# Kernel optimization log

Measured on AMD Instinct MI355X. Metric: run time of the kernel, lower is better.

The kernel has to match this reference:

```python
import jax, jax.numpy as jnp
import numpy as np

# dims
B, L, HID, TDIM, LT = 8, 4096, 1024, 768, 77
DIM = 512            # vmamba_dim
D_INNER = 2 * DIM    # expand = 2
NHEADS = DIM // 16   # 32
HEADDIM = D_INNER // NHEADS  # 32
D_STATE = 64
CONV_K = 4
CONV_DIM = D_INNER + 2 * D_STATE  # 1152
D_PROJ = 2 * D_INNER + 2 * D_STATE + NHEADS  # z | xBC | dt


def setup_inputs() -> dict:
    key = jax.random.key(0)
    ks = jax.random.split(key, 20)
    s = 0.02
    return {
        "image_tokens": jax.random.normal(ks[0], (B, L, HID), jnp.float32),
        "text_tokens": jax.random.normal(ks[1], (B, LT, TDIM), jnp.float32),
        "W_in": jax.random.normal(ks[2], (HID, DIM), jnp.float32) * s,
        "b_in": jnp.zeros((DIM,), jnp.float32),
        "W_txt": jax.random.normal(ks[3], (TDIM, DIM), jnp.float32) * s,
        "b_txt": jnp.zeros((DIM,), jnp.float32),
        "norm_w": jnp.ones((DIM,), jnp.float32),
        "norm_b": jnp.zeros((DIM,), jnp.float32),
        "W_zxbcdt": jax.random.normal(ks[4], (DIM, D_PROJ), jnp.float32) * s,
        "b_zxbcdt": jnp.zeros((D_PROJ,), jnp.float32),
        "conv_w": jax.random.normal(ks[5], (CONV_DIM, CONV_K), jnp.float32) * 0.1,
        "conv_b": jnp.zeros((CONV_DIM,), jnp.float32),
        "dt_bias": jax.random.uniform(ks[6], (NHEADS,), jnp.float32, -4.0, -2.0),
        "A_log": jnp.log(jnp.arange(1, NHEADS + 1, dtype=jnp.float32)),
        "D": jnp.ones((NHEADS,), jnp.float32),
        "W_blk_out": jax.random.normal(ks[7], (D_INNER, DIM), jnp.float32) * s,
        "b_blk_out": jnp.zeros((DIM,), jnp.float32),
        "W_out": jax.random.normal(ks[8], (DIM, HID), jnp.float32) * s,
        "b_out": jnp.zeros((HID,), jnp.float32),
    }


def _layernorm(x, w, b, eps=1e-5):
    mu = x.mean(-1, keepdims=True)
    var = ((x - mu) ** 2).mean(-1, keepdims=True)
    return (x - mu) * jax.lax.rsqrt(var + eps) * w + b


def _mamba2_block(tok, norm_w, norm_b, W_zxbcdt, b_zxbcdt, conv_w, conv_b,
                  dt_bias, A_log, Dp, W_blk_out, b_blk_out):
    x = _layernorm(tok, norm_w, norm_b)
    zxbcdt = x @ W_zxbcdt + b_zxbcdt                       # [B,L,D_PROJ]
    z = zxbcdt[..., :D_INNER]
    xBC = zxbcdt[..., D_INNER:D_INNER + CONV_DIM]
    dt = zxbcdt[..., D_INNER + CONV_DIM:]                  # [B,L,H]
    # causal depthwise conv1d, kernel 4
    xp = jnp.pad(xBC, ((0, 0), (CONV_K - 1, 0), (0, 0)))
    conv = sum(xp[:, k:k + L, :] * conv_w[None, None, :, k] for k in range(CONV_K))
    xBC = jax.nn.silu(conv + conv_b)
    xh = xBC[..., :D_INNER].reshape(B, L, NHEADS, HEADDIM)  # [B,L,H,P]
    Bm = xBC[..., D_INNER:D_INNER + D_STATE]                # [B,L,N]
    Cm = xBC[..., D_INNER + D_STATE:]                       # [B,L,N]
    dt = jax.nn.softplus(dt + dt_bias)                      # [B,L,H]
    A = -jnp.exp(A_log)                                     # [H]
    dA = jnp.exp(dt * A)                                    # [B,L,H]

    def step(h, xs):
        dA_t, dt_t, B_t, C_t, x_t = xs   # [B,H],[B,H],[B,N],[B,N],[B,H,P]
        h = h * dA_t[:, :, None, None] + \
            (dt_t[:, :, None, None] * x_t[..., None]) * B_t[:, None, None, :]
        y = jnp.einsum('bhpn,bn->bhp', h, C_t)
        return h, y

    xs = (dA.transpose(1, 0, 2), dt.transpose(1, 0, 2),
          Bm.transpose(1, 0, 2), Cm.transpose(1, 0, 2),
          xh.transpose(1, 0, 2, 3))
    h0 = jnp.zeros((B, NHEADS, HEADDIM, D_STATE), tok.dtype)
    _, ys = jax.lax.scan(step, h0, xs)                      # [L,B,H,P]
    y = ys.transpose(1, 0, 2, 3) + Dp[None, None, :, None] * xh
    y = y.reshape(B, L, D_INNER) * jax.nn.silu(z)
    return tok + (y @ W_blk_out + b_blk_out)                # residual


def reference(image_tokens, text_tokens, W_in, b_in, W_txt, b_txt,
              norm_w, norm_b, W_zxbcdt, b_zxbcdt, conv_w, conv_b,
              dt_bias, A_log, D, W_blk_out, b_blk_out, W_out, b_out):
    txt = text_tokens[:, 0, :] @ W_txt + b_txt              # cls pool
    tok = image_tokens @ W_in + b_in + txt[:, None, :]
    tok = _mamba2_block(tok, norm_w, norm_b, W_zxbcdt, b_zxbcdt, conv_w,
                        conv_b, dt_bias, A_log, D, W_blk_out, b_blk_out)
    tok = tok @ W_out + b_out                               # [B,L,HID]
    return tok.mean(axis=1)                                 # AdaptiveAvgPool1d(1)
```

## Files before the change

### kernel.cpp

```cpp
#include <hip/hip_runtime.h>

typedef unsigned short U16;
typedef __attribute__((ext_vector_type(2))) float f32x2;
typedef __attribute__((ext_vector_type(4))) float f32x4;
typedef __attribute__((ext_vector_type(8))) short short8;
typedef __attribute__((ext_vector_type(8))) __bf16 bf16x8;

#define Bsz 8
#define Lsz 4096
#define HID 1024
#define DIMV 512
#define D_INNER 1024
#define NHEADS 32
#define HEADDIM 32
#define D_STATE 64
#define CONV_DIM 1152
#define D_PROJ 2208
#define D_PROJ_PAD 2304
#define MROWS 32768
#define CL2 512
#define NSUB 8
#define NCH 8

__device__ __forceinline__ float bf2f(U16 u) {
  return __builtin_bit_cast(float, (unsigned)(((unsigned)u) << 16));
}
__device__ __forceinline__ U16 f2bf(float f) {
  unsigned u = __builtin_bit_cast(unsigned, f);
  return (U16)((u + 0x7FFFu + ((u >> 16) & 1u)) >> 16);
}
__device__ __forceinline__ void gload_lds16(const void* g, void* l) {
  __builtin_amdgcn_global_load_lds((const __attribute__((address_space(1))) unsigned int*)g,
                                   (__attribute__((address_space(3))) unsigned int*)l, 16, 0, 0);
}

__global__ __launch_bounds__(512) void txt_kernel(const float* __restrict__ text,
                                                  const float* __restrict__ Wt,
                                                  const float* __restrict__ bt,
                                                  float* __restrict__ txt) {
  int b = blockIdx.x, j = threadIdx.x;
  float s = bt[j];
  const float* tp = text + (size_t)b * 77 * 768;
  for (int k = 0; k < 768; ++k) s += tp[k] * Wt[(size_t)k * 512 + j];
  txt[b * 512 + j] = s;
}

__global__ __launch_bounds__(256) void cvt_f2b_kernel(const float* __restrict__ in,
                                                      U16* __restrict__ out, int n4) {
  int i = blockIdx.x * 256 + threadIdx.x;
  if (i < n4) {
    float4 v = reinterpret_cast<const float4*>(in)[i];
    ushort4 o;
    o.x = f2bf(v.x); o.y = f2bf(v.y); o.z = f2bf(v.z); o.w = f2bf(v.w);
    reinterpret_cast<ushort4*>(out)[i] = o;
  }
}

__global__ __launch_bounds__(256) void transpose_cvt_kernel(const float* __restrict__ in,
                                                            U16* __restrict__ out,
                                                            int K, int N, int Npad) {
  __shared__ U16 tile[32][33];
  int n0 = blockIdx.x * 32, k0 = blockIdx.y * 32;
  int tx = threadIdx.x, ty = threadIdx.y;
  #pragma unroll
  for (int i = 0; i < 4; ++i) {
    int k = k0 + ty + i * 8, n = n0 + tx;
    float v = (n < N) ? in[(size_t)k * N + n] : 0.f;
    tile[ty + i * 8][tx] = f2bf(v);
  }
  __syncthreads();
  #pragma unroll
  for (int i = 0; i < 4; ++i) {
    int n = n0 + ty + i * 8;
    out[(size_t)n * K + k0 + tx] = tile[tx][ty + i * 8];
  }
}

template <int EPI>
__global__ __launch_bounds__(256) void gemm_kernel(const U16* __restrict__ A,
                                                   const U16* __restrict__ Bt,
                                                   U16* __restrict__ C,
                                                   const float* __restrict__ bias,
                                                   const float* __restrict__ txtv,
                                                   int M, int K, int Nreal) {
  __shared__ alignas(16) U16 As[128 * 64];
  __shared__ alignas(16) U16 Bs[128 * 64];
  const int tid = threadIdx.x;
  const int wid = tid >> 6, lane = tid & 63;
  const int lhi = lane >> 4, llo = lane & 15;
  const int m0 = blockIdx.x * 128;
  const int n0 = blockIdx.y * 128;
  const int wr = wid >> 1, wc = wid & 1;
  f32x4 acc[4][4] = {};

  for (int k0 = 0; k0 < K; k0 += 64) {
    __syncthreads();
    #pragma unroll
    for (int is = 0; is < 4; ++is) {
      int qbase = is * 256 + wid * 64;
      int q = qbase + lane;
      int r = q >> 3;
      int cc = (q & 7) ^ (r & 7);
      gload_lds16(A + (size_t)(m0 + r) * K + k0 + cc * 8, &As[qbase * 8]);
    }
    #pragma unroll
    for (int is = 0; is < 4; ++is) {
      int qbase = is * 256 + wid * 64;
      int q = qbase + lane;
      int r = q >> 3;
      int cc = (q & 7) ^ (r & 7);
      gload_lds16(Bt + (size_t)(n0 + r) * K + k0 + cc * 8, &Bs[qbase * 8]);
    }
    __syncthreads();
    #pragma unroll
    for (int kk = 0; kk < 64; kk += 32) {
      bf16x8 av[4], bv[4];
      #pragma unroll
      for (int i = 0; i < 4; ++i) {
        int ra = wr * 64 + i * 16 + llo;
        short8 a = *reinterpret_cast<const short8*>(
            &As[ra * 64 + ((((kk >> 3) + lhi) ^ (ra & 7)) << 3)]);
        av[i] = __builtin_bit_cast(bf16x8, a);
        int rb = wc * 64 + i * 16 + llo;
        short8 b = *reinterpret_cast<const short8*>(
            &Bs[rb * 64 + ((((kk >> 3) + lhi) ^ (rb & 7)) << 3)]);
        bv[i] = __builtin_bit_cast(bf16x8, b);
      }
      #pragma unroll
      for (int i = 0; i < 4; ++i)
        #pragma unroll
        for (int j = 0; j < 4; ++j)
          acc[i][j] = __builtin_amdgcn_mfma_f32_16x16x32_bf16(av[i], bv[j], acc[i][j], 0, 0, 0);
    }
  }
  const int b = m0 >> 12;
  #pragma unroll
  for (int i = 0; i < 4; ++i) {
    int rbase = m0 + wr * 64 + i * 16 + lhi * 4;
    #pragma unroll
    for (int j = 0; j < 4; ++j) {
      int cg = n0 + wc * 64 + j * 16 + llo;
      if (cg < Nreal) {
        float badd = bias[cg] + (EPI ? txtv[b * 512 + cg] : 0.f);
        #pragma unroll
        for (int r = 0; r < 4; ++r)
          C[(size_t)(rbase + r) * Nreal + cg] = f2bf(acc[i][j][r] + badd);
      }
    }
  }
}

__global__ __launch_bounds__(128) void ln_kernel(const U16* __restrict__ tok,
                                                 U16* __restrict__ xo,
                                                 const float* __restrict__ w,
                                                 const float* __restrict__ bb) {
  int row = blockIdx.x, tid = threadIdx.x;
  const U16* rp = tok + (size_t)row * 512 + tid * 4;
  uint2 raw = *reinterpret_cast<const uint2*>(rp);
  float f0 = bf2f((U16)(raw.x & 0xffff)), f1 = bf2f((U16)(raw.x >> 16));
  float f2 = bf2f((U16)(raw.y & 0xffff)), f3 = bf2f((U16)(raw.y >> 16));
  float s = f0 + f1 + f2 + f3;
  float q = f0 * f0 + f1 * f1 + f2 * f2 + f3 * f3;
  for (int m = 1; m < 64; m <<= 1) { s += __shfl_xor(s, m); q += __shfl_xor(q, m); }
  __shared__ float ss[2], qq[2];
  if ((tid & 63) == 0) { ss[tid >> 6] = s; qq[tid >> 6] = q; }
  __syncthreads();
  s = ss[0] + ss[1]; q = qq[0] + qq[1];
  float mu = s * (1.f / 512.f);
  float var = q * (1.f / 512.f) - mu * mu;
  float rs = rsqrtf(var + 1e-5f);
  int j0 = tid * 4;
  unsigned c0 = f2bf((f0 - mu) * rs * w[j0] + bb[j0]);
  unsigned c1 = f2bf((f1 - mu) * rs * w[j0 + 1] + bb[j0 + 1]);
  unsigned c2 = f2bf((f2 - mu) * rs * w[j0 + 2] + bb[j0 + 2]);
  unsigned c3 = f2bf((f3 - mu) * rs * w[j0 + 3] + bb[j0 + 3]);
  uint2 o; o.x = c0 | (c1 << 16); o.y = c2 | (c3 << 16);
  *reinterpret_cast<uint2*>(xo + (size_t)row * 512 + j0) = o;
}

__global__ __launch_bounds__(256) void tokpart_kernel(const U16* __restrict__ tok,
                                                      float* __restrict__ part) {
  int b = blockIdx.x, j = blockIdx.y * 256 + threadIdx.x, z = blockIdx.z;
  float s = 0.f;
  int l0 = z * 256;
  for (int l = l0; l < l0 + 256; ++l)
    s += bf2f(tok[((size_t)b * Lsz + l) * 512 + j]);
  part[(z * 8 + b) * 512 + j] = s;
}

__global__ __launch_bounds__(256) void dt_kernel(const U16* __restrict__ zx,
                                                 const float* __restrict__ dt_bias,
                                                 const float* __restrict__ A_log,
                                                 float* __restrict__ ldt2f,
                                                 float* __restrict__ ldA2f) {
  int idx = blockIdx.x * 256 + threadIdx.x;
  int row = idx >> 5, hh = idx & 31;
  float raw = bf2f(zx[(size_t)row * D_PROJ + 2176 + hh]) + dt_bias[hh];
  float dt = (raw > 20.f) ? raw : log1pf(__expf(raw));
  float A = -__expf(A_log[hh]);
  ldt2f[idx] = __log2f(dt);
  ldA2f[idx] = dt * A * 1.44269504088896f;
}

__global__ __launch_bounds__(256) void conv_tr_kernel(
    const U16* __restrict__ zx, const float* __restrict__ cw,
    const float* __restrict__ cb, U16* __restrict__ Bmo, U16* __restrict__ Cmo,
    U16* __restrict__ xh_t, U16* __restrict__ gz_t,
    U16* __restrict__ bm_t, U16* __restrict__ cm_t) {
  __shared__ U16 tile[64 * 72];
  const int lt = blockIdx.x, ct = blockIdx.y;
  const int r0 = lt * 64;
  const int b = r0 >> 12, l0 = r0 & 4095;
  const int tid = threadIdx.x;
  const int c = tid & 63, lqb = tid >> 6;

  if (ct < 16) {
    const int zc0 = ct * 64;
    #pragma unroll
    for (int it = 0; it < 4; ++it) {
      int lq4 = (lqb + it * 4) * 4;
      float v[4];
      #pragma unroll
      for (int j = 0; j < 4; ++j) {
        float z = bf2f(zx[(size_t)(r0 + lq4 + j) * D_PROJ + zc0 + c]);
        v[j] = z / (1.f + __expf(-z));
      }
      uint2 p2;
      p2.x = (unsigned)f2bf(v[0]) | ((unsigned)f2bf(v[1]) << 16);
      p2.y = (unsigned)f2bf(v[2]) | ((unsigned)f2bf(v[3]) << 16);
      *reinterpret_cast<uint2*>(reinterpret_cast<char*>(tile) + (size_t)c * 144 + lq4 * 2) = p2;
    }
    __syncthreads();
    int c2 = tid >> 2, seg = tid & 3;
    const char* src = reinterpret_cast<const char*>(tile) + (size_t)c2 * 144 + seg * 32;
    f32x4 a = *reinterpret_cast<const f32x4*>(src);
    f32x4 bq = *reinterpret_cast<const f32x4*>(src + 16);
    U16* dst = gz_t + ((size_t)b * 1024 + zc0 + c2) * 4096 + l0 + seg * 16;
    *reinterpret_cast<f32x4*>(dst) = a;
    *reinterpret_cast<f32x4*>(dst + 8) = bq;
  } else {
    const int cc = (ct - 16) * 64 + c;
    const float4 w4 = *reinterpret_cast<const float4*>(cw + cc * 4);
    const float cbv = cb[cc];
    #pragma unroll
    for (int it = 0; it < 4; ++it) {
      int lq4 = (lqb + it * 4) * 4;
      float v7[7];
      #pragma unroll
      for (int k = 0; k < 7; ++k) {
        int lrel = lq4 + k - 3;
        v7[k] = (l0 + lrel >= 0)
                    ? bf2f(zx[(size_t)(r0 + lrel) * D_PROJ + D_INNER + cc])
                    : 0.f;
      }
      float o[4];
      #pragma unroll
      for (int j = 0; j < 4; ++j) {
        float acc = cbv + v7[j] * w4.x + v7[j + 1] * w4.y + v7[j + 2] * w4.z + v7[j + 3] * w4.w;
        o[j] = acc / (1.f + __expf(-acc));
      }
      uint2 p2;
      p2.x = (unsigned)f2bf(o[0]) | ((unsigned)f2bf(o[1]) << 16);
      p2.y = (unsigned)f2bf(o[2]) | ((unsigned)f2bf(o[3]) << 16);
      *reinterpret_cast<uint2*>(reinterpret_cast<char*>(tile) + (size_t)c * 144 + lq4 * 2) = p2;
      if (cc >= 1024) {
        U16* outp = (cc < 1088) ? Bmo : Cmo;
        int n = cc & 63;
        #pragma unroll
        for (int j = 0; j < 4; ++j)
          outp[(size_t)(r0 + lq4 + j) * 64 + n] = f2bf(o[j]);
      }
    }
    __syncthreads();
    int c2 = tid >> 2, seg = tid & 3;
    const char* src = reinterpret_cast<const char*>(tile) + (size_t)c2 * 144 + seg * 32;
    f32x4 a = *reinterpret_cast<const f32x4*>(src);
    f32x4 bq = *reinterpret_cast<const f32x4*>(src + 16);
    int cc2 = (ct - 16) * 64 + c2;
    U16* dst;
    if (cc2 < 1024)      dst = xh_t + ((size_t)b * 1024 + cc2) * 4096 + l0 + seg * 16;
    else if (cc2 < 1088) dst = bm_t + ((size_t)(b * 64 + cc2 - 1024)) * 4096 + l0 + seg * 16;
    else                 dst = cm_t + ((size_t)(b * 64 + cc2 - 1088)) * 4096 + l0 + seg * 16;
    *reinterpret_cast<f32x4*>(dst) = a;
    *reinterpret_cast<f32x4*>(dst + 8) = bq;
  }
}

__global__ __launch_bounds__(64, 2) void scan_chunk_kernel(
    const U16* __restrict__ xh_t, const U16* __restrict__ gz_t,
    const U16* __restrict__ Bm, const U16* __restrict__ Cm,
    const U16* __restrict__ bm_t, const U16* __restrict__ cm_t,
    const float* __restrict__ ldt2f, const float* __restrict__ ldA2f,
    const float* __restrict__ Dp,
    float* __restrict__ hpart, float* __restrict__ wacc,
    float* __restrict__ ylocal, float* __restrict__ aprod) {
  const int bx = blockIdx.x;
  const int hh = bx & 31, ci = (bx >> 5) & 7, b = bx >> 8;
  const int l = threadIdx.x;
  const int tl = l & 15, lg = l >> 4;

  __shared__ U16 Msm[64 * 72];
  __shared__ float qsm[64], la2sm[64], casm[64], cfsm[64];
  __shared__ float ysm[32];

  #pragma unroll
  for (int i = 0; i < 9; ++i)
    *reinterpret_cast<f32x4*>(reinterpret_cast<char*>(Msm) + (size_t)l * 144 + i * 16) =
        f32x4{0.f, 0.f, 0.f, 0.f};
  __syncthreads();

  f32x4 hC[2][4] = {};
  f32x4 WB[2][4] = {};
  float corrv[2][4] = {};
  float ylac[2] = {0.f, 0.f}, dxac[2] = {0.f, 0.f};
  float capfx = 1.f;
  const size_t xgrow = ((size_t)b * 1024 + hh * 32) * 4096;

  for (int sc = 0; sc < NSUB; ++sc) {
    const int lglob = ci * CL2 + sc * 64;
    const int r0g = b * 4096 + lglob;

    float ldA2 = ldA2f[(size_t)(r0g + l) * 32 + hh];
    float ldt2 = ldt2f[(size_t)(r0g + l) * 32 + hh];
    float la = ldA2;
    #pragma unroll
    for (int d = 1; d < 64; d <<= 1) {
      float o = __shfl_up(la, d);
      if (l >= d) la += o;
    }
    float laend = __shfl(la, 63);
    qsm[l] = ldt2 - la;
    la2sm[l] = la;
    casm[l] = exp2f(la);
    cfsm[l] = exp2f(laend + ldt2 - la);
    __syncthreads();

    f32x4 g[10];
    #pragma unroll
    for (int i = 0; i < 10; ++i) g[i] = f32x4{0.f, 0.f, 0.f, 0.f};
    #pragma unroll
    for (int k = 0; k < 2; ++k) {
      bf16x8 af[4], cf4[4];
      #pragma unroll
      for (int si = 0; si < 4; ++si)
        af[si] = *reinterpret_cast<const bf16x8*>(
            Bm + (size_t)(r0g + si * 16 + tl) * 64 + k * 32 + lg * 8);
      #pragma unroll
      for (int ti = 0; ti < 4; ++ti)
        cf4[ti] = *reinterpret_cast<const bf16x8*>(
            Cm + (size_t)(r0g + ti * 16 + tl) * 64 + k * 32 + lg * 8);
      int idx = 0;
      #pragma unroll
      for (int si = 0; si < 4; ++si)
        #pragma unroll
        for (int ti = si; ti < 4; ++ti) {
          g[idx] = __builtin_amdgcn_mfma_f32_16x16x32_bf16(af[si], cf4[ti], g[idx], 0, 0, 0);
          ++idx;
        }
    }

    {
      int idx = 0;
      #pragma unroll
      for (int si = 0; si < 4; ++si) {
        f32x4 q4 = *reinterpret_cast<const f32x4*>(&qsm[si * 16 + lg * 4]);
        #pragma unroll
        for (int ti = si; ti < 4; ++ti) {
          float lat = la2sm[ti * 16 + tl];
          f32x4 gv = g[idx]; ++idx;
          float v[4];
          #pragma unroll
          for (int r = 0; r < 4; ++r) {
            float val = gv[r] * exp2f(lat + q4[r]);
            if (si == ti) val = (lg * 4 + r <= tl) ? val : 0.f;
            v[r] = val;
          }
          uint2 pk;
          pk.x = (unsigned)f2bf(v[0]) | ((unsigned)f2bf(v[1]) << 16);
          pk.y = (unsigned)f2bf(v[2]) | ((unsigned)f2bf(v[3]) << 16);
          *reinterpret_cast<uint2*>(reinterpret_cast<char*>(Msm) +
                                    (size_t)(ti * 16 + tl) * 144 + (size_t)(si * 16 + lg * 4) * 2) = pk;
        }
      }
    }
    __syncthreads();

    {
      bf16x8 xb[2][2];
      #pragma unroll
      for (int pt = 0; pt < 2; ++pt)
        #pragma unroll
        for (int ks = 0; ks < 2; ++ks)
          xb[pt][ks] = *reinterpret_cast<const bf16x8*>(
              xh_t + xgrow + (size_t)(pt * 16 + tl) * 4096 + lglob + ks * 32 + lg * 8);
      #pragma unroll
      for (int tt = 0; tt < 4; ++tt) {
        f32x4 y[2] = {f32x4{0.f, 0.f, 0.f, 0.f}, f32x4{0.f, 0.f, 0.f, 0.f}};
        #pragma unroll
        for (int ks = 0; ks < 2; ++ks) {
          bf16x8 mf = *reinterpret_cast<const bf16x8*>(
              reinterpret_cast<char*>(Msm) + (size_t)(tt * 16 + tl) * 144 + (ks * 32 + lg * 8) * 2);
          #pragma unroll
          for (int pt = 0; pt < 2; ++pt)
            y[pt] = __builtin_amdgcn_mfma_f32_16x16x32_bf16(mf, xb[pt][ks], y[pt], 0, 0, 0);
        }
        #pragma unroll
        for (int pt = 0; pt < 2; ++pt) {
          size_t ro = xgrow + (size_t)(pt * 16 + tl) * 4096 + lglob + tt * 16 + lg * 4;
          uint2 gz2 = *reinterpret_cast<const uint2*>(gz_t + ro);
          uint2 xx2 = *reinterpret_cast<const uint2*>(xh_t + ro);
          float gzv[4] = {bf2f((U16)(gz2.x & 0xffff)), bf2f((U16)(gz2.x >> 16)),
                          bf2f((U16)(gz2.y & 0xffff)), bf2f((U16)(gz2.y >> 16))};
          float xxv[4] = {bf2f((U16)(xx2.x & 0xffff)), bf2f((U16)(xx2.x >> 16)),
                          bf2f((U16)(xx2.y & 0xffff)), bf2f((U16)(xx2.y >> 16))};
          #pragma unroll
          for (int r = 0; r < 4; ++r) {
            ylac[pt] = fmaf(gzv[r], y[pt][r], ylac[pt]);
            dxac[pt] = fmaf(gzv[r], xxv[r], dxac[pt]);
          }
        }
      }
    }

    bf16x8 ga[2][2], xa[2][2];
    #pragma unroll
    for (int pt = 0; pt < 2; ++pt)
      #pragma unroll
      for (int kt = 0; kt < 2; ++kt) {
        size_t ro = xgrow + (size_t)(pt * 16 + tl) * 4096 + lglob + kt * 32 + lg * 8;
        short8 graw = *reinterpret_cast<const short8*>(gz_t + ro);
        short8 xraw = *reinterpret_cast<const short8*>(xh_t + ro);
        const float* cap = &casm[kt * 32 + lg * 8];
        const float* cfp = &cfsm[kt * 32 + lg * 8];
        short8 gs, xs8;
        #pragma unroll
        for (int j = 0; j < 8; ++j) {
          gs[j] = (short)f2bf(bf2f((U16)graw[j]) * cap[j]);
          xs8[j] = (short)f2bf(bf2f((U16)xraw[j]) * cfp[j]);
        }
        ga[pt][kt] = __builtin_bit_cast(bf16x8, gs);
        xa[pt][kt] = __builtin_bit_cast(bf16x8, xs8);
      }
    f32x4 ws[2][4] = {};
    f32x4 hs[2][4] = {};
    #pragma unroll
    for (int kt = 0; kt < 2; ++kt) {
      bf16x8 cbf[4], bbf[4];
      #pragma unroll
      for (int nt = 0; nt < 4; ++nt) {
        cbf[nt] = *reinterpret_cast<const bf16x8*>(
            cm_t + (size_t)(b * 64 + nt * 16 + tl) * 4096 + lglob + kt * 32 + lg * 8);
        bbf[nt] = *reinterpret_cast<const bf16x8*>(
            bm_t + (size_t)(b * 64 + nt * 16 + tl) * 4096 + lglob + kt * 32 + lg * 8);
      }
      #pragma unroll
      for (int pt = 0; pt < 2; ++pt)
        #pragma unroll
        for (int nt = 0; nt < 4; ++nt) {
          ws[pt][nt] = __builtin_amdgcn_mfma_f32_16x16x32_bf16(ga[pt][kt], cbf[nt], ws[pt][nt], 0, 0, 0);
          hs[pt][nt] = __builtin_amdgcn_mfma_f32_16x16x32_bf16(xa[pt][kt], bbf[nt], hs[pt][nt], 0, 0, 0);
        }
    }

    float cs = exp2f(laend);
    #pragma unroll
    for (int pt = 0; pt < 2; ++pt) {
      f32x4 a4 = hC[pt][0] * ws[pt][0] + hC[pt][1] * ws[pt][1] +
                 hC[pt][2] * ws[pt][2] + hC[pt][3] * ws[pt][3];
      #pragma unroll
      for (int r = 0; r < 4; ++r) {
        float cc = a4[r];
        cc += __shfl_xor(cc, 1); cc += __shfl_xor(cc, 2);
        cc += __shfl_xor(cc, 4); cc += __shfl_xor(cc, 8);
        corrv[pt][r] += cc;
      }
      #pragma unroll
      for (int nt = 0; nt < 4; ++nt) {
        WB[pt][nt] = WB[pt][nt] + ws[pt][nt] * capfx;
        hC[pt][nt] = hC[pt][nt] * cs + hs[pt][nt];
      }
    }
    capfx *= cs;
    __syncthreads();
  }

  #pragma unroll
  for (int pt = 0; pt < 2; ++pt)
    #pragma unroll
    for (int nt = 0; nt < 4; ++nt) {
      size_t slot = (size_t)bx * 2048 + (size_t)((pt * 4 + nt) * 64 + l) * 4;
      *reinterpret_cast<f32x4*>(hpart + slot) = hC[pt][nt];
      *reinterpret_cast<f32x4*>(wacc + slot) = WB[pt][nt];
    }
  const float Dh = Dp[hh];
  #pragma unroll
  for (int pt = 0; pt < 2; ++pt) {
    float yv = ylac[pt] + Dh * dxac[pt];
    yv += __shfl_xor(yv, 16);
    yv += __shfl_xor(yv, 32);
    if (l < 16) ysm[pt * 16 + l] = yv;
  }
  __syncthreads();
  if (tl == 0) {
    #pragma unroll
    for (int pt = 0; pt < 2; ++pt)
      #pragma unroll
      for (int r = 0; r < 4; ++r)
        ysm[pt * 16 + lg * 4 + r] += corrv[pt][r];
  }
  __syncthreads();
  if (l < 32) ylocal[(size_t)bx * 32 + l] = ysm[l];
  if (l == 0) aprod[bx] = capfx;
}

__global__ __launch_bounds__(64) void scan_combine_kernel(
    const float* __restrict__ hpart, const float* __restrict__ wacc,
    const float* __restrict__ ylocal, const float* __restrict__ aprod,
    float* __restrict__ yysum) {
  const int bh = blockIdx.x;
  const int b = bh >> 5, hh = bh & 31;
  const int l = threadIdx.x, tl = l & 15, lg = l >> 4;
  __shared__ float ysm[32];
  f32x4 hr[8] = {};
  float cv[8] = {};
  float ylsum = 0.f;
  for (int ci = 0; ci < NCH; ++ci) {
    int bx = (b * NCH + ci) * 32 + hh;
    size_t base = (size_t)bx * 2048 + (size_t)l * 4;
    f32x4 w[8], p[8];
    #pragma unroll
    for (int t8 = 0; t8 < 8; ++t8) {
      w[t8] = *reinterpret_cast<const f32x4*>(wacc + base + t8 * 256);
      p[t8] = *reinterpret_cast<const f32x4*>(hpart + base + t8 * 256);
    }
    float ap = aprod[bx];
    #pragma unroll
    for (int pt = 0; pt < 2; ++pt) {
      f32x4 a4 = hr[pt * 4] * w[pt * 4] + hr[pt * 4 + 1] * w[pt * 4 + 1] +
                 hr[pt * 4 + 2] * w[pt * 4 + 2] + hr[pt * 4 + 3] * w[pt * 4 + 3];
      #pragma unroll
      for (int r = 0; r < 4; ++r) cv[pt * 4 + r] += a4[r];
    }
    #pragma unroll
    for (int t8 = 0; t8 < 8; ++t8) hr[t8] = hr[t8] * ap + p[t8];
    if (l < 32) ylsum += ylocal[(size_t)bx * 32 + l];
  }
  #pragma unroll
  for (int i = 0; i < 8; ++i) {
    cv[i] += __shfl_xor(cv[i], 1); cv[i] += __shfl_xor(cv[i], 2);
    cv[i] += __shfl_xor(cv[i], 4); cv[i] += __shfl_xor(cv[i], 8);
  }
  if (l < 32) ysm[l] = ylsum;
  __syncthreads();
  if (tl == 0) {
    #pragma unroll
    for (int pt = 0; pt < 2; ++pt)
      #pragma unroll
      for (int r = 0; r < 4; ++r)
        ysm[pt * 16 + lg * 4 + r] += cv[pt * 4 + r];
  }
  __syncthreads();
  if (l < 32) yysum[(size_t)b * 1024 + hh * 32 + l] = ysm[l];
}

__global__ __launch_bounds__(128) void final1_kernel(const float* __restrict__ tokpart,
                                                     const float* __restrict__ yysum,
                                                     const float* __restrict__ Wb,
                                                     const float* __restrict__ bb,
                                                     float* __restrict__ m2) {
  int b = blockIdx.x, j = blockIdx.y * 128 + threadIdx.x;
  float tm = 0.f;
  #pragma unroll
  for (int z = 0; z < 16; ++z) tm += tokpart[(z * 8 + b) * 512 + j];
  float s = 0.f;
  for (int d = 0; d < 1024; ++d) s += yysum[b * 1024 + d] * Wb[(size_t)d * 512 + j];
  m2[b * 512 + j] = (tm + s) * (1.f / (float)Lsz) + bb[j];
}

__global__ __launch_bounds__(256) void final2_kernel(const float* __restrict__ m2,
                                                     const float* __restrict__ Wo,
                                                     const float* __restrict__ bo,
                                                     float* __restrict__ out) {
  int b = blockIdx.x, o = blockIdx.y * 256 + threadIdx.x;
  float s = 0.f;
  for (int j = 0; j < 512; ++j) s += m2[b * 512 + j] * Wo[(size_t)j * 1024 + o];
  out[b * 1024 + o] = s + bo[o];
}

extern "C" void kernel_launch(void* const* d_in, const int* in_sizes, int n_in,
                              void* d_out, int out_size, void* d_ws, size_t ws_size,
                              hipStream_t stream) {
  const float* image = (const float*)d_in[0];
  const float* text = (const float*)d_in[1];
  const float* W_in = (const float*)d_in[2];
  const float* b_in = (const float*)d_in[3];
  const float* W_txt = (const float*)d_in[4];
  const float* b_txt = (const float*)d_in[5];
  const float* norm_w = (const float*)d_in[6];
  const float* norm_b = (const float*)d_in[7];
  const float* W_zx = (const float*)d_in[8];
  const float* b_zx = (const float*)d_in[9];
  const float* conv_w = (const float*)d_in[10];
  const float* conv_b = (const float*)d_in[11];
  const float* dt_bias = (const float*)d_in[12];
  const float* A_log = (const float*)d_in[13];
  const float* Dp = (const float*)d_in[14];
  const float* W_blk = (const float*)d_in[15];
  const float* b_blk = (const float*)d_in[16];
  const float* W_out = (const float*)d_in[17];
  const float* b_out = (const float*)d_in[18];
  float* out = (float*)d_out;

  char* ws = (char*)d_ws;
  size_t off = 0;
  auto take = [&](size_t bytes) {
    char* p = ws + off;
    off = (off + bytes + 255) & ~(size_t)255;
    return p;
  };
  U16* img_bf = (U16*)take((size_t)MROWS * HID * 2);
  U16* wt_in = (U16*)take((size_t)DIMV * HID * 2);
  U16* wt_zx = (U16*)take((size_t)D_PROJ_PAD * DIMV * 2);
  U16* tok_bf = (U16*)take((size_t)MROWS * DIMV * 2);
  U16* x_bf = (U16*)take((size_t)MROWS * DIMV * 2);
  U16* zx_bf = (U16*)take((size_t)MROWS * D_PROJ * 2);
  U16* xh_t = (U16*)take((size_t)MROWS * D_INNER * 2);
  U16* bm_bf = (U16*)take((size_t)MROWS * 64 * 2);
  U16* cm_bf = (U16*)take((size_t)MROWS * 64 * 2);
  U16* bm_t = (U16*)take((size_t)MROWS * 64 * 2);
  U16* cm_t = (U16*)take((size_t)MROWS * 64 * 2);
  float* ldt2f = (float*)take((size_t)MROWS * 32 * 4);
  float* ldA2f = (float*)take((size_t)MROWS * 32 * 4);
  float* txtf = (float*)take(8 * 512 * 4);
  float* tokpart = (float*)take(16 * 8 * 512 * 4);
  float* yysum = (float*)take(8 * 1024 * 4);
  float* m2 = (float*)take(8 * 512 * 4);
  float* ylocal = (float*)take((size_t)2048 * 32 * 4);
  float* aprod = (float*)take((size_t)2048 * 4);
  U16* gz_t = img_bf;
  float* hpart = (float*)tok_bf;
  float* wacc = (float*)x_bf;

  txt_kernel<<<8, 512, 0, stream>>>(text, W_txt, b_txt, txtf);
  cvt_f2b_kernel<<<(MROWS * HID / 4 + 255) / 256, 256, 0, stream>>>(image, img_bf, MROWS * HID / 4);
  transpose_cvt_kernel<<<dim3(DIMV / 32, HID / 32), dim3(32, 8), 0, stream>>>(W_in, wt_in, HID, DIMV, DIMV);
  transpose_cvt_kernel<<<dim3(D_PROJ_PAD / 32, DIMV / 32), dim3(32, 8), 0, stream>>>(W_zx, wt_zx, DIMV, D_PROJ, D_PROJ_PAD);

  gemm_kernel<1><<<dim3(MROWS / 128, DIMV / 128), 256, 0, stream>>>(img_bf, wt_in, tok_bf, b_in, txtf, MROWS, HID, DIMV);
  tokpart_kernel<<<dim3(8, 2, 16), 256, 0, stream>>>(tok_bf, tokpart);
  ln_kernel<<<MROWS, 128, 0, stream>>>(tok_bf, x_bf, norm_w, norm_b);

  gemm_kernel<0><<<dim3(MROWS / 128, D_PROJ_PAD / 128), 256, 0, stream>>>(x_bf, wt_zx, zx_bf, b_zx, nullptr, MROWS, DIMV, D_PROJ);

  dt_kernel<<<MROWS * 32 / 256, 256, 0, stream>>>(zx_bf, dt_bias, A_log, ldt2f, ldA2f);
  conv_tr_kernel<<<dim3(MROWS / 64, 34), 256, 0, stream>>>(zx_bf, conv_w, conv_b, bm_bf, cm_bf,
                                                           xh_t, gz_t, bm_t, cm_t);

  scan_chunk_kernel<<<8 * NCH * 32, 64, 0, stream>>>(xh_t, gz_t, bm_bf, cm_bf, bm_t, cm_t,
                                                     ldt2f, ldA2f, Dp, hpart, wacc, ylocal, aprod);
  scan_combine_kernel<<<256, 64, 0, stream>>>(hpart, wacc, ylocal, aprod, yysum);

  final1_kernel<<<dim3(8, 4), 128, 0, stream>>>(tokpart, yysum, W_blk, b_blk, m2);
  final2_kernel<<<dim3(8, 4), 256, 0, stream>>>(m2, W_out, b_out, out);
}
```

Measured before the change: 635.0 us.

## Fuse fp32-to-bf16 conversion into GEMM, precompute scan decays, pack scan blocks

The first GEMM now reads the fp32 image directly and converts it to bf16 while staging into LDS, which removes the separate conversion kernel and its 64MB bf16 round trip. The dt kernel is replaced by a decay kernel that also does the per-subchunk prefix sum and the exp2 terms, writing a packed float4 per position. The scan kernel consumes these precomputed values and packs four independent single-wave units into each 256-thread block, dropping its barriers. In exchange, the A operand of the first GEMM now goes through register loads instead of direct-to-LDS loads, and the decay buffer is larger than the two arrays it replaces.

```diff
diff --git a/kernel.cpp b/kernel.cpp
--- a/kernel.cpp
+++ b/kernel.cpp
@@ -45,17 +45,6 @@
   txt[b * 512 + j] = s;
 }
 
-__global__ __launch_bounds__(256) void cvt_f2b_kernel(const float* __restrict__ in,
-                                                      U16* __restrict__ out, int n4) {
-  int i = blockIdx.x * 256 + threadIdx.x;
-  if (i < n4) {
-    float4 v = reinterpret_cast<const float4*>(in)[i];
-    ushort4 o;
-    o.x = f2bf(v.x); o.y = f2bf(v.y); o.z = f2bf(v.z); o.w = f2bf(v.w);
-    reinterpret_cast<ushort4*>(out)[i] = o;
-  }
-}
-
 __global__ __launch_bounds__(256) void transpose_cvt_kernel(const float* __restrict__ in,
                                                             U16* __restrict__ out,
                                                             int K, int N, int Npad) {
@@ -76,8 +65,8 @@
   }
 }
 
-template <int EPI>
-__global__ __launch_bounds__(256) void gemm_kernel(const U16* __restrict__ A,
+template <int EPI, int AF32>
+__global__ __launch_bounds__(256) void gemm_kernel(const void* __restrict__ Ap,
                                                    const U16* __restrict__ Bt,
                                                    U16* __restrict__ C,
                                                    const float* __restrict__ bias,
@@ -95,13 +84,34 @@
 
   for (int k0 = 0; k0 < K; k0 += 64) {
     __syncthreads();
-    #pragma unroll
-    for (int is = 0; is < 4; ++is) {
-      int qbase = is * 256 + wid * 64;
-      int q = qbase + lane;
-      int r = q >> 3;
-      int cc = (q & 7) ^ (r & 7);
-      gload_lds16(A + (size_t)(m0 + r) * K + k0 + cc * 8, &As[qbase * 8]);
+    if constexpr (AF32) {
+      const float* Af = (const float*)Ap;
+      #pragma unroll
+      for (int is = 0; is < 4; ++is) {
+        int q = is * 256 + tid;
+        int r = q >> 3, cl = q & 7;
+        int cg = cl ^ (r & 7);
+        const float* src = Af + (size_t)(m0 + r) * K + k0 + cg * 8;
+        f32x4 v0 = *reinterpret_cast<const f32x4*>(src);
+        f32x4 v1 = *reinterpret_cast<const f32x4*>(src + 4);
+        short8 o;
+        #pragma unroll
+        for (int j = 0; j < 4; ++j) {
+          o[j] = (short)f2bf(v0[j]);
+          o[j + 4] = (short)f2bf(v1[j]);
+        }
+        *reinterpret_cast<short8*>(&As[q * 8]) = o;
+      }
+    } else {
+      const U16* A = (const U16*)Ap;
+      #pragma unroll
+      for (int is = 0; is < 4; ++is) {
+        int qbase = is * 256 + wid * 64;
+        int q = qbase + lane;
+        int r = q >> 3;
+        int cc = (q & 7) ^ (r & 7);
+        gload_lds16(A + (size_t)(m0 + r) * K + k0 + cc * 8, &As[qbase * 8]);
+      }
     }
     #pragma unroll
     for (int is = 0; is < 4; ++is) {
@@ -188,18 +198,32 @@
   part[(z * 8 + b) * 512 + j] = s;
 }
 
-__global__ __launch_bounds__(256) void dt_kernel(const U16* __restrict__ zx,
-                                                 const float* __restrict__ dt_bias,
-                                                 const float* __restrict__ A_log,
-                                                 float* __restrict__ ldt2f,
-                                                 float* __restrict__ ldA2f) {
-  int idx = blockIdx.x * 256 + threadIdx.x;
-  int row = idx >> 5, hh = idx & 31;
-  float raw = bf2f(zx[(size_t)row * D_PROJ + 2176 + hh]) + dt_bias[hh];
-  float dt = (raw > 20.f) ? raw : log1pf(__expf(raw));
-  float A = -__expf(A_log[hh]);
-  ldt2f[idx] = __log2f(dt);
-  ldA2f[idx] = dt * A * 1.44269504088896f;
+__global__ __launch_bounds__(256) void decay_kernel(const U16* __restrict__ zx,
+                                                    const float* __restrict__ dt_bias,
+                                                    const float* __restrict__ A_log,
+                                                    float* __restrict__ decay4) {
+  const int sc = blockIdx.x;
+  const int w = threadIdx.x >> 6, l = threadIdx.x & 63;
+  const int r0 = sc * 64;
+  const int b = r0 >> 12, l0 = r0 & 4095;
+  #pragma unroll
+  for (int i = 0; i < 8; ++i) {
+    int hh = w * 8 + i;
+    float raw = bf2f(zx[(size_t)(r0 + l) * D_PROJ + 2176 + hh]) + dt_bias[hh];
+    float dt = (raw > 20.f) ? raw : log1pf(__expf(raw));
+    float A = -__expf(A_log[hh]);
+    float ldA2 = dt * A * 1.44269504088896f;
+    float ldt2 = __log2f(dt);
+    float la = ldA2;
+    #pragma unroll
+    for (int d = 1; d < 64; d <<= 1) {
+      float o = __shfl_up(la, d);
+      if (l >= d) la += o;
+    }
+    float laend = __shfl(la, 63);
+    f32x4 v = {ldt2 - la, la, exp2f(la), exp2f(laend + ldt2 - la)};
+    *reinterpret_cast<f32x4*>(decay4 + ((size_t)(b * 32 + hh) * 4096 + l0 + l) * 4) = v;
+  }
 }
 
 __global__ __launch_bounds__(256) void conv_tr_kernel(
@@ -286,28 +310,30 @@
   }
 }
 
-__global__ __launch_bounds__(64, 2) void scan_chunk_kernel(
+__global__ __launch_bounds__(256, 3) void scan_chunk_kernel(
     const U16* __restrict__ xh_t, const U16* __restrict__ gz_t,
     const U16* __restrict__ Bm, const U16* __restrict__ Cm,
     const U16* __restrict__ bm_t, const U16* __restrict__ cm_t,
-    const float* __restrict__ ldt2f, const float* __restrict__ ldA2f,
-    const float* __restrict__ Dp,
+    const float* __restrict__ decay4, const float* __restrict__ Dp,
     float* __restrict__ hpart, float* __restrict__ wacc,
     float* __restrict__ ylocal, float* __restrict__ aprod) {
-  const int bx = blockIdx.x;
-  const int hh = bx & 31, ci = (bx >> 5) & 7, b = bx >> 8;
-  const int l = threadIdx.x;
+  const int w = threadIdx.x >> 6, l = threadIdx.x & 63;
+  const int u = blockIdx.x * 4 + w;
+  const int hh = u & 31, ci = (u >> 5) & 7, b = u >> 8;
   const int tl = l & 15, lg = l >> 4;
 
-  __shared__ U16 Msm[64 * 72];
-  __shared__ float qsm[64], la2sm[64], casm[64], cfsm[64];
-  __shared__ float ysm[32];
+  __shared__ alignas(16) U16 MsmAll[4 * 64 * 72];
+  __shared__ alignas(16) float decAll[4 * 256];
+  U16* Msm = &MsmAll[w * 64 * 72];
+  float* qsm = &decAll[w * 256];
+  float* la2sm = qsm + 64;
+  float* casm = qsm + 128;
+  float* cfsm = qsm + 192;
 
   #pragma unroll
   for (int i = 0; i < 9; ++i)
     *reinterpret_cast<f32x4*>(reinterpret_cast<char*>(Msm) + (size_t)l * 144 + i * 16) =
         f32x4{0.f, 0.f, 0.f, 0.f};
-  __syncthreads();
 
   f32x4 hC[2][4] = {};
   f32x4 WB[2][4] = {};
@@ -315,25 +341,17 @@
   float ylac[2] = {0.f, 0.f}, dxac[2] = {0.f, 0.f};
   float capfx = 1.f;
   const size_t xgrow = ((size_t)b * 1024 + hh * 32) * 4096;
+  const float* dbase = decay4 + ((size_t)(b * 32 + hh) * 4096) * 4;
 
   for (int sc = 0; sc < NSUB; ++sc) {
     const int lglob = ci * CL2 + sc * 64;
     const int r0g = b * 4096 + lglob;
 
-    float ldA2 = ldA2f[(size_t)(r0g + l) * 32 + hh];
-    float ldt2 = ldt2f[(size_t)(r0g + l) * 32 + hh];
-    float la = ldA2;
-    #pragma unroll
-    for (int d = 1; d < 64; d <<= 1) {
-      float o = __shfl_up(la, d);
-      if (l >= d) la += o;
-    }
-    float laend = __shfl(la, 63);
-    qsm[l] = ldt2 - la;
-    la2sm[l] = la;
-    casm[l] = exp2f(la);
-    cfsm[l] = exp2f(laend + ldt2 - la);
-    __syncthreads();
+    f32x4 dv = *reinterpret_cast<const f32x4*>(dbase + (size_t)(lglob + l) * 4);
+    qsm[l] = dv[0];
+    la2sm[l] = dv[1];
+    casm[l] = dv[2];
+    cfsm[l] = dv[3];
 
     f32x4 g[10];
     #pragma unroll
@@ -383,7 +401,6 @@
         }
       }
     }
-    __syncthreads();
 
     {
       bf16x8 xb[2][2];
@@ -462,7 +479,7 @@
         }
     }
 
-    float cs = exp2f(laend);
+    float cs = casm[63];
     #pragma unroll
     for (int pt = 0; pt < 2; ++pt) {
       f32x4 a4 = hC[pt][0] * ws[pt][0] + hC[pt][1] * ws[pt][1] +
@@ -481,18 +498,18 @@
       }
     }
     capfx *= cs;
-    __syncthreads();
   }
 
   #pragma unroll
   for (int pt = 0; pt < 2; ++pt)
     #pragma unroll
     for (int nt = 0; nt < 4; ++nt) {
-      size_t slot = (size_t)bx * 2048 + (size_t)((pt * 4 + nt) * 64 + l) * 4;
+      size_t slot = (size_t)u * 2048 + (size_t)((pt * 4 + nt) * 64 + l) * 4;
       *reinterpret_cast<f32x4*>(hpart + slot) = hC[pt][nt];
       *reinterpret_cast<f32x4*>(wacc + slot) = WB[pt][nt];
     }
   const float Dh = Dp[hh];
+  float* ysm = qsm;
   #pragma unroll
   for (int pt = 0; pt < 2; ++pt) {
     float yv = ylac[pt] + Dh * dxac[pt];
@@ -500,7 +517,6 @@
     yv += __shfl_xor(yv, 32);
     if (l < 16) ysm[pt * 16 + l] = yv;
   }
-  __syncthreads();
   if (tl == 0) {
     #pragma unroll
     for (int pt = 0; pt < 2; ++pt)
@@ -508,9 +524,8 @@
       for (int r = 0; r < 4; ++r)
         ysm[pt * 16 + lg * 4 + r] += corrv[pt][r];
   }
-  __syncthreads();
-  if (l < 32) ylocal[(size_t)bx * 32 + l] = ysm[l];
-  if (l == 0) aprod[bx] = capfx;
+  if (l < 32) ylocal[(size_t)u * 32 + l] = ysm[l];
+  if (l == 0) aprod[u] = capfx;
 }
 
 __global__ __launch_bounds__(64) void scan_combine_kernel(
@@ -618,7 +633,7 @@
     off = (off + bytes + 255) & ~(size_t)255;
     return p;
   };
-  U16* img_bf = (U16*)take((size_t)MROWS * HID * 2);
+  U16* gz_t = (U16*)take((size_t)MROWS * HID * 2);
   U16* wt_in = (U16*)take((size_t)DIMV * HID * 2);
   U16* wt_zx = (U16*)take((size_t)D_PROJ_PAD * DIMV * 2);
   U16* tok_bf = (U16*)take((size_t)MROWS * DIMV * 2);
@@ -629,35 +644,34 @@
   U16* cm_bf = (U16*)take((size_t)MROWS * 64 * 2);
   U16* bm_t = (U16*)take((size_t)MROWS * 64 * 2);
   U16* cm_t = (U16*)take((size_t)MROWS * 64 * 2);
-  float* ldt2f = (float*)take((size_t)MROWS * 32 * 4);
-  float* ldA2f = (float*)take((size_t)MROWS * 32 * 4);
+  float* decay4 = (float*)take((size_t)256 * 4096 * 16);
   float* txtf = (float*)take(8 * 512 * 4);
   float* tokpart = (float*)take(16 * 8 * 512 * 4);
   float* yysum = (float*)take(8 * 1024 * 4);
   float* m2 = (float*)take(8 * 512 * 4);
   float* ylocal = (float*)take((size_t)2048 * 32 * 4);
   float* aprod = (float*)take((size_t)2048 * 4);
-  U16* gz_t = img_bf;
   float* hpart = (float*)tok_bf;
   float* wacc = (float*)x_bf;
 
   txt_kernel<<<8, 512, 0, stream>>>(text, W_txt, b_txt, txtf);
-  cvt_f2b_kernel<<<(MROWS * HID / 4 + 255) / 256, 256, 0, stream>>>(image, img_bf, MROWS * HID / 4);
   transpose_cvt_kernel<<<dim3(DIMV / 32, HID / 32), dim3(32, 8), 0, stream>>>(W_in, wt_in, HID, DIMV, DIMV);
   transpose_cvt_kernel<<<dim3(D_PROJ_PAD / 32, DIMV / 32), dim3(32, 8), 0, stream>>>(W_zx, wt_zx, DIMV, D_PROJ, D_PROJ_PAD);
 
-  gemm_kernel<1><<<dim3(MROWS / 128, DIMV / 128), 256, 0, stream>>>(img_bf, wt_in, tok_bf, b_in, txtf, MROWS, HID, DIMV);
+  gemm_kernel<1, 1><<<dim3(MROWS / 128, DIMV / 128), 256, 0, stream>>>(
+      (const void*)image, wt_in, tok_bf, b_in, txtf, MROWS, HID, DIMV);
   tokpart_kernel<<<dim3(8, 2, 16), 256, 0, stream>>>(tok_bf, tokpart);
   ln_kernel<<<MROWS, 128, 0, stream>>>(tok_bf, x_bf, norm_w, norm_b);
 
-  gemm_kernel<0><<<dim3(MROWS / 128, D_PROJ_PAD / 128), 256, 0, stream>>>(x_bf, wt_zx, zx_bf, b_zx, nullptr, MROWS, DIMV, D_PROJ);
-
-  dt_kernel<<<MROWS * 32 / 256, 256, 0, stream>>>(zx_bf, dt_bias, A_log, ldt2f, ldA2f);
+  gemm_kernel<0, 0><<<dim3(MROWS / 128, D_PROJ_PAD / 128), 256, 0, stream>>>(
+      (const void*)x_bf, wt_zx, zx_bf, b_zx, nullptr, MROWS, DIMV, D_PROJ);
+
+  decay_kernel<<<512, 256, 0, stream>>>(zx_bf, dt_bias, A_log, decay4);
   conv_tr_kernel<<<dim3(MROWS / 64, 34), 256, 0, stream>>>(zx_bf, conv_w, conv_b, bm_bf, cm_bf,
                                                            xh_t, gz_t, bm_t, cm_t);
 
-  scan_chunk_kernel<<<8 * NCH * 32, 64, 0, stream>>>(xh_t, gz_t, bm_bf, cm_bf, bm_t, cm_t,
-                                                     ldt2f, ldA2f, Dp, hpart, wacc, ylocal, aprod);
+  scan_chunk_kernel<<<512, 256, 0, stream>>>(xh_t, gz_t, bm_bf, cm_bf, bm_t, cm_t,
+                                             decay4, Dp, hpart, wacc, ylocal, aprod);
   scan_combine_kernel<<<256, 64, 0, stream>>>(hpart, wacc, ylocal, aprod, yysum);
 
   final1_kernel<<<dim3(8, 4), 128, 0, stream>>>(tokpart, yysum, W_blk, b_blk, m2);
```

Result: slower. 764.3 us (+20.3%).
